# Optimization experiments

Hardware: AMD Instinct MI355X
Metric: run time of the kernel (lower is better)

## Reference

```python
import jax, jax.numpy as jnp
import numpy as np
from jax import lax

EPS = 1e-5
W_BITS = 8
A_BITS = 8


def _ste_round(x):
    # straight-through round (brevitas-style)
    return x + lax.stop_gradient(jnp.round(x) - x)


def weight_fake_quant(w, bits=W_BITS):
    # symmetric per-output-channel int quant: scale = max|w| / (2^(b-1)-1)
    qmax = float(2 ** (bits - 1) - 1)
    s = jnp.max(jnp.abs(w), axis=(1, 2, 3), keepdims=True) / qmax
    s = jnp.maximum(s, 1e-8)
    return jnp.clip(_ste_round(w / s), -qmax, qmax) * s


def quant_relu(x, scale, bits=A_BITS):
    # QuantReLU: relu then unsigned fake-quant with learned per-tensor scale
    qmax = float(2 ** bits - 1)
    s = jnp.maximum(scale, 1e-6)
    return jnp.clip(_ste_round(jax.nn.relu(x) / s), 0.0, qmax) * s


def conv2d(x, w, stride=1, padding=0):
    return lax.conv_general_dilated(
        x, w, window_strides=(stride, stride),
        padding=[(padding, padding), (padding, padding)],
        dimension_numbers=('NCHW', 'OIHW', 'NCHW'))


def batchnorm(x, gamma, beta, mean, var):
    # eval-mode BN with running stats
    inv = gamma / jnp.sqrt(var + EPS)
    return x * inv[None, :, None, None] + (beta - mean * inv)[None, :, None, None]


def setup_inputs() -> dict:
    key = jax.random.key(0)
    ks = jax.random.split(key, 20)
    B, Cin, P, H, W = 64, 1024, 256, 14, 14
    inp = {
        'x': jax.random.normal(ks[0], (B, Cin, H, W), jnp.float32),
        'w1': jax.random.normal(ks[1], (P, Cin, 1, 1), jnp.float32) * 0.05,
        'w2': jax.random.normal(ks[2], (P, P, 3, 3), jnp.float32) * 0.05,
        'w3': jax.random.normal(ks[3], (Cin, P, 1, 1), jnp.float32) * 0.05,
        'bn1_gamma': jax.random.uniform(ks[4], (P,), jnp.float32, 0.5, 1.5),
        'bn1_beta': jax.random.normal(ks[5], (P,), jnp.float32) * 0.1,
        'bn1_mean': jax.random.normal(ks[6], (P,), jnp.float32) * 0.1,
        'bn1_var': jax.random.uniform(ks[7], (P,), jnp.float32, 0.5, 1.5),
        'bn2_gamma': jax.random.uniform(ks[8], (P,), jnp.float32, 0.5, 1.5),
        'bn2_beta': jax.random.normal(ks[9], (P,), jnp.float32) * 0.1,
        'bn2_mean': jax.random.normal(ks[10], (P,), jnp.float32) * 0.1,
        'bn2_var': jax.random.uniform(ks[11], (P,), jnp.float32, 0.5, 1.5),
        'bn3_gamma': jax.random.uniform(ks[12], (Cin,), jnp.float32, 0.5, 1.5),
        'bn3_beta': jax.random.normal(ks[13], (Cin,), jnp.float32) * 0.1,
        'bn3_mean': jax.random.normal(ks[14], (Cin,), jnp.float32) * 0.1,
        'bn3_var': jax.random.uniform(ks[15], (Cin,), jnp.float32, 0.5, 1.5),
        's1': jax.random.uniform(ks[16], (1,), jnp.float32, 0.02, 0.1),
        's2': jax.random.uniform(ks[17], (1,), jnp.float32, 0.02, 0.1),
        's3': jax.random.uniform(ks[18], (1,), jnp.float32, 0.02, 0.1),
    }
    return inp


def reference(x, w1, w2, w3,
              bn1_gamma, bn1_beta, bn1_mean, bn1_var,
              bn2_gamma, bn2_beta, bn2_mean, bn2_var,
              bn3_gamma, bn3_beta, bn3_mean, bn3_var,
              s1, s2, s3):
    identity = x
    out = conv2d(x, weight_fake_quant(w1))
    out = batchnorm(out, bn1_gamma, bn1_beta, bn1_mean, bn1_var)
    out = quant_relu(out, s1)
    out = conv2d(out, weight_fake_quant(w2), stride=1, padding=1)
    out = batchnorm(out, bn2_gamma, bn2_beta, bn2_mean, bn2_var)
    out = quant_relu(out, s2)
    out = conv2d(out, weight_fake_quant(w3))
    out = batchnorm(out, bn3_gamma, bn3_beta, bn3_mean, bn3_var)
    out = out + identity  # downsample=None -> identity skip
    out = quant_relu(out, s3)
    return out
```

## Files before the change

### kernel.cpp

```cpp
#include <hip/hip_runtime.h>
#include <stdint.h>
#include <stddef.h>

typedef unsigned short u16;
typedef unsigned int   u32;
typedef __bf16  bf16x8 __attribute__((ext_vector_type(8)));
typedef unsigned short us8 __attribute__((ext_vector_type(8)));
typedef unsigned short us4 __attribute__((ext_vector_type(4)));
typedef float   f32x4  __attribute__((ext_vector_type(4)));

#define DEVFN static __device__ __forceinline__

DEVFN u16 f2bf(float f) {
    u32 u = __float_as_uint(f);
    return (u16)((u + 0x7FFFu + ((u >> 16) & 1u)) >> 16);
}
DEVFN float bf2f(u16 h) { return __uint_as_float(((u32)h) << 16); }

#define GLL(g, l) __builtin_amdgcn_global_load_lds( \
    (__attribute__((address_space(1))) void*)(g),   \
    (__attribute__((address_space(3))) void*)(l), 16, 0, 0)

#define NREAL 12544
#define NPAD  16384
#define GUARD_ROWS 32

DEVFN float blockReduceMax(float m) {
    for (int off = 32; off; off >>= 1) m = fmaxf(m, __shfl_xor(m, off));
    __shared__ float s[4];
    int lane = threadIdx.x & 63, w = threadIdx.x >> 6;
    if (lane == 0) s[w] = m;
    __syncthreads();
    m = fmaxf(fmaxf(s[0], s[1]), fmaxf(s[2], s[3]));
    return m;
}

__global__ __launch_bounds__(256) void k_prep(
    const float* __restrict__ w1, const float* __restrict__ w2, const float* __restrict__ w3,
    const float* __restrict__ x,
    u16* __restrict__ w1d, u16* __restrict__ w2t, u16* __restrict__ w3q,
    float* __restrict__ sw1, float* __restrict__ sw2, float* __restrict__ sw3,
    u16* __restrict__ xsplit)
{
    __shared__ float tile[64*197];
    const int bid = blockIdx.x, t = threadIdx.x;

    if (bid < 256) {
        int p = bid;
        const float* wr = w1 + (size_t)p * 1024;
        float v[4], m = 0.f;
        for (int i = 0; i < 4; ++i) { v[i] = wr[t + i*256]; m = fmaxf(m, fabsf(v[i])); }
        m = blockReduceMax(m);
        float s = fmaxf(m / 127.0f, 1e-8f);
        if (t == 0) sw1[p] = s;
        for (int i = 0; i < 4; ++i) {
            float q = rintf(v[i] / s);
            q = fminf(fmaxf(q, -127.f), 127.f);
            u16 h = f2bf(q);
            w1d[(size_t)p*2048 + t + i*256]        = h;
            w1d[(size_t)p*2048 + 1024 + t + i*256] = h;
        }
    } else if (bid < 512) {
        int p = bid - 256;
        const float* wr = w2 + (size_t)p * 2304;
        float v[9], m = 0.f;
        for (int i = 0; i < 9; ++i) { v[i] = wr[t + i*256]; m = fmaxf(m, fabsf(v[i])); }
        m = blockReduceMax(m);
        float s = fmaxf(m / 127.0f, 1e-8f);
        if (t == 0) sw2[p] = s;
        for (int i = 0; i < 9; ++i) {
            int f = t + i*256;
            int ci = f / 9, r = f - ci*9;
            float q = rintf(v[i] / s);
            q = fminf(fmaxf(q, -127.f), 127.f);
            w2t[(size_t)p*2304 + r*256 + ci] = f2bf(q);
        }
    } else if (bid < 1536) {
        int co = bid - 512;
        float v = w3[(size_t)co*256 + t];
        float m = blockReduceMax(fabsf(v));
        float s = fmaxf(m / 127.0f, 1e-8f);
        if (t == 0) sw3[co] = s;
        float q = rintf(v / s);
        q = fminf(fmaxf(q, -127.f), 127.f);
        w3q[(size_t)co*256 + t] = f2bf(q);
    } else {
        int sb = bid - 1536;
        int b = sb >> 4, cg = sb & 15;
        const float* xb = x + ((size_t)b*1024 + cg*64) * 196;
        for (int i = t; i < 3136; i += 256) {
            f32x4 v = *(const f32x4*)&xb[i*4];
            int g = i*4;
#pragma unroll
            for (int j = 0; j < 4; ++j) {
                int gg = g + j;
                tile[gg + gg/196] = v[j];
            }
        }
        __syncthreads();
        for (int i = t; i < 3136; i += 256) {
            int pos = i >> 4, c4 = (i & 15) << 2;
            us4 hi, lo;
#pragma unroll
            for (int j = 0; j < 4; ++j) {
                float v = tile[(c4 + j)*197 + pos];
                u16 h = f2bf(v);
                hi[j] = h;
                lo[j] = f2bf(v - bf2f(h));
            }
            size_t n = (size_t)(b*196 + pos);
            *(us4*)&xsplit[n*2048 + cg*64 + c4]        = hi;
            *(us4*)&xsplit[n*2048 + 1024 + cg*64 + c4] = lo;
        }
    }
}

__global__ void k_coef(const float* g1, const float* b1, const float* m1, const float* v1,
                       const float* g2, const float* b2, const float* m2, const float* v2,
                       const float* g3, const float* b3, const float* m3, const float* v3,
                       const float* s1p, const float* s2p,
                       const float* sw1, const float* sw2, const float* sw3,
                       float* a1, float* c1, float* a2, float* c2, float* a3, float* c3) {
    int t = threadIdx.x;
    float s1 = fmaxf(s1p[0], 1e-6f), s2 = fmaxf(s2p[0], 1e-6f);
    if (t < 256) {
        float inv1 = g1[t] / sqrtf(v1[t] + 1e-5f);
        a1[t] = sw1[t] * inv1 / s1;
        c1[t] = (b1[t] - m1[t] * inv1) / s1;
        float inv2 = g2[t] / sqrtf(v2[t] + 1e-5f);
        a2[t] = sw2[t] * s1 * inv2 / s2;
        c2[t] = (b2[t] - m2[t] * inv2) / s2;
    }
    float inv3 = g3[t] / sqrtf(v3[t] + 1e-5f);
    a3[t] = sw3[t] * s2 * inv3;
    c3[t] = b3[t] - m3[t] * inv3;
}

template<int CONV>
__global__ __launch_bounds__(256) void k_gemm(
    const u16* __restrict__ A, const u16* __restrict__ Bact,
    u16* __restrict__ actout,
    const float* __restrict__ ca, const float* __restrict__ cc,
    const float* __restrict__ xin, const float* __restrict__ s3p,
    float* __restrict__ outp)
{
    constexpr int KSA = CONV==1 ? 2048 : (CONV==2 ? 2304 : 256);
    constexpr int KSB = CONV==1 ? 2048 : 256;
    constexpr int NKT = CONV==1 ? 32 : (CONV==2 ? 36 : 4);

    __shared__ u16 lA[3][128*64];
    __shared__ u16 lB[3][64*64];

    const int t = threadIdx.x;
    const int lane = t & 63, wv = t >> 6;
    const int n0 = blockIdx.x * 64, m0 = blockIdx.y * 128;

    f32x4 acc[4][2];
#pragma unroll
    for (int i = 0; i < 4; ++i)
#pragma unroll
        for (int j = 0; j < 2; ++j) acc[i][j] = f32x4{0.f,0.f,0.f,0.f};

    const int srA = wv*32 + (lane >> 3);
    const int srB = wv*16 + (lane >> 3);
    const int ssel = (((lane & 7) ^ ((lane >> 3) & 7))) * 8;
    const int wr = wv >> 1, wc = wv & 1;
    const int fr = lane & 15, fg = lane >> 4;
    const int fsw = (fr & 7) << 4;

    auto stageK = [&](int kt, int buf) {
        int bcol, bshift;
        if constexpr (CONV == 2) {
            bcol = (kt & 3) * 64;
            int kpos = kt >> 2;
            int ky = kpos / 3, kx = kpos - ky*3;
            bshift = (ky - 1)*16 + (kx - 1);
        } else { bcol = kt * 64; bshift = 0; }
#pragma unroll
        for (int c = 0; c < 4; ++c) {
            const u16* g = A + (size_t)(m0 + srA + c*8) * KSA + kt*64 + ssel;
            GLL(g, &lA[buf][(wv*32 + c*8) * 64]);
        }
#pragma unroll
        for (int c = 0; c < 2; ++c) {
            const u16* g = Bact + (ptrdiff_t)(n0 + srB + c*8 + bshift) * KSB + bcol + ssel;
            GLL(g, &lB[buf][(wv*16 + c*8) * 64]);
        }
    };

    auto computeK = [&](int buf) {
        const char* bA = (const char*)&lA[buf][0];
        const char* bB = (const char*)&lB[buf][0];
        __builtin_amdgcn_s_setprio(1);
#pragma unroll
        for (int kk = 0; kk < 2; ++kk) {
            bf16x8 af[4], bfv[2];
#pragma unroll
            for (int m = 0; m < 4; ++m) {
                int row = wr*64 + m*16 + fr;
                const char* p = bA + row*128 + ((kk*64 + fg*16) ^ fsw);
                af[m] = __builtin_bit_cast(bf16x8, *(const us8*)p);
            }
#pragma unroll
            for (int n = 0; n < 2; ++n) {
                int row = wc*32 + n*16 + fr;
                const char* p = bB + row*128 + ((kk*64 + fg*16) ^ fsw);
                bfv[n] = __builtin_bit_cast(bf16x8, *(const us8*)p);
            }
#pragma unroll
            for (int m = 0; m < 4; ++m)
#pragma unroll
                for (int n = 0; n < 2; ++n)
                    acc[m][n] = __builtin_amdgcn_mfma_f32_16x16x32_bf16(af[m], bfv[n], acc[m][n], 0, 0, 0);
        }
        __builtin_amdgcn_s_setprio(0);
    };

    stageK(0, 0);
    stageK(1, 1);
    asm volatile("s_waitcnt vmcnt(6)" ::: "memory");
    __builtin_amdgcn_s_barrier();

    int cur = 0;
    for (int kt = 0; kt < NKT; ++kt) {
        int nxt2 = cur + 2; if (nxt2 >= 3) nxt2 -= 3;
        if (kt + 2 < NKT) stageK(kt + 2, nxt2);
        computeK(cur);
        if (kt + 1 < NKT) {
            if (kt + 2 < NKT) { asm volatile("s_waitcnt vmcnt(6)" ::: "memory"); }
            else              { asm volatile("s_waitcnt vmcnt(0)" ::: "memory"); }
            __builtin_amdgcn_s_barrier();
        }
        cur = cur + 1 == 3 ? 0 : cur + 1;
    }

    const int pb = m0 + wr*64 + fg*4;
    const int nb = n0 + wc*32 + fr;

    if constexpr (CONV != 3) {
        (void)xin; (void)s3p; (void)outp;
#pragma unroll
        for (int m = 0; m < 4; ++m) {
            int p0 = pb + m*16;
            float av[4], cv[4];
#pragma unroll
            for (int j = 0; j < 4; ++j) { av[j] = ca[p0+j]; cv[j] = cc[p0+j]; }
#pragma unroll
            for (int n = 0; n < 2; ++n) {
                int nn = nb + n*16;
                int np;
                if constexpr (CONV == 1) {
                    int b  = nn / 196;
                    int pos = nn - b*196;
                    int h = pos / 14, w = pos - h*14;
                    np = b*256 + (h+1)*16 + (w+1);
                } else {
                    int hp = (nn >> 4) & 15, wp = nn & 15;
                    if (hp < 1 || hp > 14 || wp < 1 || wp > 14) continue;
                    np = (nn >> 8)*196 + (hp-1)*14 + (wp-1);
                }
                us4 st;
#pragma unroll
                for (int j = 0; j < 4; ++j) {
                    float y = fmaxf(acc[m][n][j]*av[j] + cv[j], 0.f);
                    float q = fminf(rintf(y), 255.f);
                    st[j] = f2bf(q);
                }
                *(us4*)&actout[(size_t)np*256 + p0] = st;
            }
        }
    } else {
        (void)actout;
        float s3 = fmaxf(s3p[0], 1e-6f);
        float rs3 = 1.0f / s3;
#pragma unroll
        for (int n = 0; n < 2; ++n) {
            int co = nb + n*16;
            float av = ca[co], cv = cc[co];
#pragma unroll
            for (int m = 0; m < 4; ++m) {
                int p4 = pb + m*16;
                int b  = p4 / 196;
                int hw = p4 - b*196;
                size_t off = ((size_t)((b << 10) + co))*196 + hw;
                f32x4 xv = *(const f32x4*)&xin[off];
                f32x4 st;
#pragma unroll
                for (int j = 0; j < 4; ++j) {
                    float y = fmaxf(acc[m][n][j]*av + cv + xv[j], 0.f);
                    float q = fminf(rintf(y * rs3), 255.f);
                    st[j] = q * s3;
                }
                *(f32x4*)&outp[off] = st;
            }
        }
    }
}

extern "C" void kernel_launch(void* const* d_in, const int* in_sizes, int n_in,
                              void* d_out, int out_size, void* d_ws, size_t ws_size,
                              hipStream_t stream) {
    (void)in_sizes; (void)n_in; (void)out_size; (void)ws_size;
    const float* x   = (const float*)d_in[0];
    const float* w1  = (const float*)d_in[1];
    const float* w2  = (const float*)d_in[2];
    const float* w3  = (const float*)d_in[3];
    const float* g1  = (const float*)d_in[4];
    const float* b1  = (const float*)d_in[5];
    const float* m1  = (const float*)d_in[6];
    const float* v1  = (const float*)d_in[7];
    const float* g2  = (const float*)d_in[8];
    const float* b2  = (const float*)d_in[9];
    const float* m2  = (const float*)d_in[10];
    const float* v2  = (const float*)d_in[11];
    const float* g3  = (const float*)d_in[12];
    const float* b3  = (const float*)d_in[13];
    const float* m3  = (const float*)d_in[14];
    const float* v3  = (const float*)d_in[15];
    const float* s1p = (const float*)d_in[16];
    const float* s2p = (const float*)d_in[17];
    const float* s3p = (const float*)d_in[18];
    float* out = (float*)d_out;

    char* w = (char*)d_ws;
    u16* w1d = (u16*)w;  w += (size_t)256*2048*2;
    u16* w2t = (u16*)w;  w += (size_t)256*2304*2;
    u16* w3q = (u16*)w;  w += (size_t)1024*256*2;
    float* sw1 = (float*)w; w += 256*4;
    float* sw2 = (float*)w; w += 256*4;
    float* sw3 = (float*)w; w += 1024*4;
    float* a1 = (float*)w; w += 256*4;
    float* c1 = (float*)w; w += 256*4;
    float* a2 = (float*)w; w += 256*4;
    float* c2 = (float*)w; w += 256*4;
    float* a3 = (float*)w; w += 1024*4;
    float* c3 = (float*)w; w += 1024*4;
    u16* xsplit = (u16*)w; w += (size_t)NREAL*2048*2;
    u16* act1g  = (u16*)w; w += (size_t)(NPAD + 2*GUARD_ROWS)*256*2;
    u16* act1   = act1g + (size_t)GUARD_ROWS*256;
    u16* act2   = (u16*)w; w += (size_t)NREAL*256*2;

    hipMemsetAsync(act1g, 0, (size_t)(NPAD + 2*GUARD_ROWS)*256*2, stream);

    k_prep<<<2560, 256, 0, stream>>>(w1, w2, w3, x, w1d, w2t, w3q, sw1, sw2, sw3, xsplit);
    k_coef<<<1, 1024, 0, stream>>>(g1,b1,m1,v1, g2,b2,m2,v2, g3,b3,m3,v3,
                                   s1p, s2p, sw1, sw2, sw3,
                                   a1,c1, a2,c2, a3,c3);

    k_gemm<1><<<dim3(196, 2), 256, 0, stream>>>(w1d, xsplit, act1, a1, c1, nullptr, nullptr, nullptr);
    k_gemm<2><<<dim3(256, 2), 256, 0, stream>>>(w2t, act1, act2, a2, c2, nullptr, nullptr, nullptr);
    k_gemm<3><<<dim3(16, 98), 256, 0, stream>>>(act2, w3q, nullptr, a3, c3, x, s3p, out);
}
```

Baseline: 250.2 us.

## Switch all three conv GEMMs from bf16 to int8 MFMA with offset-corrected epilogues

Weights become int8 and activations are stored as offset int8 (value minus 128), with the offset folded into the BN bias using per-channel weight sums. The input x is split into fixed-point hi/lo int8 halves, and conv1 accumulates them in separate int32 accumulators. All GEMMs use the 16x16x64 i8 MFMA, halving operand bytes and K iterations. The coefficient kernel and the memset are folded into the prep kernel. The fixed-point split of x at scale 4096 with clamping adds quantization error and risks overflow for large inputs.

```diff
diff --git a/kernel.cpp b/kernel.cpp
--- a/kernel.cpp
+++ b/kernel.cpp
@@ -4,18 +4,13 @@
 
 typedef unsigned short u16;
 typedef unsigned int   u32;
-typedef __bf16  bf16x8 __attribute__((ext_vector_type(8)));
-typedef unsigned short us8 __attribute__((ext_vector_type(8)));
-typedef unsigned short us4 __attribute__((ext_vector_type(4)));
-typedef float   f32x4  __attribute__((ext_vector_type(4)));
+typedef signed char    s8;
+typedef int   i32x4 __attribute__((ext_vector_type(4)));
+typedef float f32x4 __attribute__((ext_vector_type(4)));
+typedef s8    s8x4  __attribute__((ext_vector_type(4)));
+typedef u32   u32x4 __attribute__((ext_vector_type(4)));
 
 #define DEVFN static __device__ __forceinline__
-
-DEVFN u16 f2bf(float f) {
-    u32 u = __float_as_uint(f);
-    return (u16)((u + 0x7FFFu + ((u >> 16) & 1u)) >> 16);
-}
-DEVFN float bf2f(u16 h) { return __uint_as_float(((u32)h) << 16); }
 
 #define GLL(g, l) __builtin_amdgcn_global_load_lds( \
     (__attribute__((address_space(1))) void*)(g),   \
@@ -24,6 +19,7 @@
 #define NREAL 12544
 #define NPAD  16384
 #define GUARD_ROWS 32
+#define SXI 4096.0f
 
 DEVFN float blockReduceMax(float m) {
     for (int off = 32; off; off >>= 1) m = fmaxf(m, __shfl_xor(m, off));
@@ -31,16 +27,30 @@
     int lane = threadIdx.x & 63, w = threadIdx.x >> 6;
     if (lane == 0) s[w] = m;
     __syncthreads();
-    m = fmaxf(fmaxf(s[0], s[1]), fmaxf(s[2], s[3]));
-    return m;
+    return fmaxf(fmaxf(s[0], s[1]), fmaxf(s[2], s[3]));
+}
+DEVFN float blockReduceSum(float v) {
+    for (int off = 32; off; off >>= 1) v += __shfl_xor(v, off);
+    __shared__ float s[4];
+    int lane = threadIdx.x & 63, w = threadIdx.x >> 6;
+    __syncthreads();
+    if (lane == 0) s[w] = v;
+    __syncthreads();
+    return s[0] + s[1] + s[2] + s[3];
 }
 
 __global__ __launch_bounds__(256) void k_prep(
     const float* __restrict__ w1, const float* __restrict__ w2, const float* __restrict__ w3,
     const float* __restrict__ x,
-    u16* __restrict__ w1d, u16* __restrict__ w2t, u16* __restrict__ w3q,
-    float* __restrict__ sw1, float* __restrict__ sw2, float* __restrict__ sw3,
-    u16* __restrict__ xsplit)
+    const float* __restrict__ g1, const float* __restrict__ b1, const float* __restrict__ m1, const float* __restrict__ v1,
+    const float* __restrict__ g2, const float* __restrict__ b2, const float* __restrict__ m2, const float* __restrict__ v2,
+    const float* __restrict__ g3, const float* __restrict__ b3, const float* __restrict__ m3, const float* __restrict__ v3,
+    const float* __restrict__ s1p, const float* __restrict__ s2p,
+    s8* __restrict__ w1q8, s8* __restrict__ w2t8, s8* __restrict__ w3q8,
+    float* __restrict__ a1, float* __restrict__ c1,
+    float* __restrict__ a2, float* __restrict__ c2,
+    float* __restrict__ a3, float* __restrict__ c3,
+    s8* __restrict__ xq, s8* __restrict__ act1g)
 {
     __shared__ float tile[64*197];
     const int bid = blockIdx.x, t = threadIdx.x;
@@ -48,43 +58,65 @@
     if (bid < 256) {
         int p = bid;
         const float* wr = w1 + (size_t)p * 1024;
-        float v[4], m = 0.f;
-        for (int i = 0; i < 4; ++i) { v[i] = wr[t + i*256]; m = fmaxf(m, fabsf(v[i])); }
-        m = blockReduceMax(m);
-        float s = fmaxf(m / 127.0f, 1e-8f);
-        if (t == 0) sw1[p] = s;
+        float v[4], mx = 0.f;
+        for (int i = 0; i < 4; ++i) { v[i] = wr[t + i*256]; mx = fmaxf(mx, fabsf(v[i])); }
+        mx = blockReduceMax(mx);
+        float s = fmaxf(mx / 127.0f, 1e-8f);
+        float qs = 0.f;
         for (int i = 0; i < 4; ++i) {
-            float q = rintf(v[i] / s);
-            q = fminf(fmaxf(q, -127.f), 127.f);
-            u16 h = f2bf(q);
-            w1d[(size_t)p*2048 + t + i*256]        = h;
-            w1d[(size_t)p*2048 + 1024 + t + i*256] = h;
+            float q = fminf(fmaxf(rintf(v[i] / s), -127.f), 127.f);
+            s8 qb = (s8)(int)q;
+            w1q8[(size_t)p*2048 + t + i*256]        = qb;
+            w1q8[(size_t)p*2048 + 1024 + t + i*256] = qb;
+            qs += q;
+        }
+        qs = blockReduceSum(qs);
+        if (t == 0) {
+            float s1 = fmaxf(s1p[0], 1e-6f);
+            float inv = g1[p] / sqrtf(v1[p] + 1e-5f);
+            float a = s * (1.0f / SXI) * inv / s1;
+            a1[p] = a;
+            c1[p] = (b1[p] - m1[p] * inv) / s1 + 128.0f * qs * a;
         }
     } else if (bid < 512) {
         int p = bid - 256;
         const float* wr = w2 + (size_t)p * 2304;
-        float v[9], m = 0.f;
-        for (int i = 0; i < 9; ++i) { v[i] = wr[t + i*256]; m = fmaxf(m, fabsf(v[i])); }
-        m = blockReduceMax(m);
-        float s = fmaxf(m / 127.0f, 1e-8f);
-        if (t == 0) sw2[p] = s;
+        float v[9], mx = 0.f;
+        for (int i = 0; i < 9; ++i) { v[i] = wr[t + i*256]; mx = fmaxf(mx, fabsf(v[i])); }
+        mx = blockReduceMax(mx);
+        float s = fmaxf(mx / 127.0f, 1e-8f);
+        float qs = 0.f;
         for (int i = 0; i < 9; ++i) {
             int f = t + i*256;
             int ci = f / 9, r = f - ci*9;
-            float q = rintf(v[i] / s);
-            q = fminf(fmaxf(q, -127.f), 127.f);
-            w2t[(size_t)p*2304 + r*256 + ci] = f2bf(q);
+            float q = fminf(fmaxf(rintf(v[i] / s), -127.f), 127.f);
+            w2t8[(size_t)p*2304 + r*256 + ci] = (s8)(int)q;
+            qs += q;
+        }
+        qs = blockReduceSum(qs);
+        if (t == 0) {
+            float s1 = fmaxf(s1p[0], 1e-6f), s2 = fmaxf(s2p[0], 1e-6f);
+            float inv = g2[p] / sqrtf(v2[p] + 1e-5f);
+            float a = s * s1 * inv / s2;
+            a2[p] = a;
+            c2[p] = (b2[p] - m2[p] * inv) / s2 + 128.0f * qs * a;
         }
     } else if (bid < 1536) {
         int co = bid - 512;
         float v = w3[(size_t)co*256 + t];
-        float m = blockReduceMax(fabsf(v));
-        float s = fmaxf(m / 127.0f, 1e-8f);
-        if (t == 0) sw3[co] = s;
-        float q = rintf(v / s);
-        q = fminf(fmaxf(q, -127.f), 127.f);
-        w3q[(size_t)co*256 + t] = f2bf(q);
-    } else {
+        float mx = blockReduceMax(fabsf(v));
+        float s = fmaxf(mx / 127.0f, 1e-8f);
+        float q = fminf(fmaxf(rintf(v / s), -127.f), 127.f);
+        w3q8[(size_t)co*256 + t] = (s8)(int)q;
+        float qs = blockReduceSum(q);
+        if (t == 0) {
+            float s2 = fmaxf(s2p[0], 1e-6f);
+            float inv = g3[co] / sqrtf(v3[co] + 1e-5f);
+            float a = s * s2 * inv;
+            a3[co] = a;
+            c3[co] = (b3[co] - m3[co] * inv) + 128.0f * qs * a;
+        }
+    } else if (bid < 2560) {
         int sb = bid - 1536;
         int b = sb >> 4, cg = sb & 15;
         const float* xb = x + ((size_t)b*1024 + cg*64) * 196;
@@ -100,70 +132,57 @@
         __syncthreads();
         for (int i = t; i < 3136; i += 256) {
             int pos = i >> 4, c4 = (i & 15) << 2;
-            us4 hi, lo;
+            s8x4 hi, lo;
 #pragma unroll
             for (int j = 0; j < 4; ++j) {
                 float v = tile[(c4 + j)*197 + pos];
-                u16 h = f2bf(v);
-                hi[j] = h;
-                lo[j] = f2bf(v - bf2f(h));
+                int xf = (int)rintf(v * SXI);
+                xf = xf > 32767 ? 32767 : (xf < -32767 ? -32767 : xf);
+                int h = xf >> 8;
+                int l = xf - (h << 8) - 128;
+                hi[j] = (s8)h;
+                lo[j] = (s8)l;
             }
             size_t n = (size_t)(b*196 + pos);
-            *(us4*)&xsplit[n*2048 + cg*64 + c4]        = hi;
-            *(us4*)&xsplit[n*2048 + 1024 + cg*64 + c4] = lo;
-        }
+            *(s8x4*)&xq[n*2048 + cg*64 + c4]        = hi;
+            *(s8x4*)&xq[n*2048 + 1024 + cg*64 + c4] = lo;
+        }
+    } else {
+        const int total16 = (NPAD + 2*GUARD_ROWS) * 256 / 16;
+        u32x4 val; val[0] = val[1] = val[2] = val[3] = 0x80808080u;
+        u32x4* dst = (u32x4*)act1g;
+        for (int i = (bid - 2560)*256 + t; i < total16; i += 260*256) dst[i] = val;
     }
-}
-
-__global__ void k_coef(const float* g1, const float* b1, const float* m1, const float* v1,
-                       const float* g2, const float* b2, const float* m2, const float* v2,
-                       const float* g3, const float* b3, const float* m3, const float* v3,
-                       const float* s1p, const float* s2p,
-                       const float* sw1, const float* sw2, const float* sw3,
-                       float* a1, float* c1, float* a2, float* c2, float* a3, float* c3) {
-    int t = threadIdx.x;
-    float s1 = fmaxf(s1p[0], 1e-6f), s2 = fmaxf(s2p[0], 1e-6f);
-    if (t < 256) {
-        float inv1 = g1[t] / sqrtf(v1[t] + 1e-5f);
-        a1[t] = sw1[t] * inv1 / s1;
-        c1[t] = (b1[t] - m1[t] * inv1) / s1;
-        float inv2 = g2[t] / sqrtf(v2[t] + 1e-5f);
-        a2[t] = sw2[t] * s1 * inv2 / s2;
-        c2[t] = (b2[t] - m2[t] * inv2) / s2;
-    }
-    float inv3 = g3[t] / sqrtf(v3[t] + 1e-5f);
-    a3[t] = sw3[t] * s2 * inv3;
-    c3[t] = b3[t] - m3[t] * inv3;
 }
 
 template<int CONV>
 __global__ __launch_bounds__(256) void k_gemm(
-    const u16* __restrict__ A, const u16* __restrict__ Bact,
-    u16* __restrict__ actout,
+    const s8* __restrict__ A, const s8* __restrict__ Bact,
+    s8* __restrict__ actout,
     const float* __restrict__ ca, const float* __restrict__ cc,
     const float* __restrict__ xin, const float* __restrict__ s3p,
     float* __restrict__ outp)
 {
     constexpr int KSA = CONV==1 ? 2048 : (CONV==2 ? 2304 : 256);
     constexpr int KSB = CONV==1 ? 2048 : 256;
-    constexpr int NKT = CONV==1 ? 32 : (CONV==2 ? 36 : 4);
-
-    __shared__ u16 lA[3][128*64];
-    __shared__ u16 lB[3][64*64];
+    constexpr int NKT = CONV==1 ? 16 : (CONV==2 ? 18 : 2);
+
+    __shared__ s8 lA[3][128*128];
+    __shared__ s8 lB[3][64*128];
 
     const int t = threadIdx.x;
     const int lane = t & 63, wv = t >> 6;
     const int n0 = blockIdx.x * 64, m0 = blockIdx.y * 128;
 
-    f32x4 acc[4][2];
+    i32x4 acc[4][2], accB[4][2];
 #pragma unroll
     for (int i = 0; i < 4; ++i)
 #pragma unroll
-        for (int j = 0; j < 2; ++j) acc[i][j] = f32x4{0.f,0.f,0.f,0.f};
+        for (int j = 0; j < 2; ++j) { acc[i][j] = i32x4{0,0,0,0}; accB[i][j] = i32x4{0,0,0,0}; }
 
     const int srA = wv*32 + (lane >> 3);
     const int srB = wv*16 + (lane >> 3);
-    const int ssel = (((lane & 7) ^ ((lane >> 3) & 7))) * 8;
+    const int ssel = (((lane & 7) ^ ((lane >> 3) & 7))) * 16;
     const int wr = wv >> 1, wc = wv & 1;
     const int fr = lane & 15, fg = lane >> 4;
     const int fsw = (fr & 7) << 4;
@@ -171,47 +190,45 @@
     auto stageK = [&](int kt, int buf) {
         int bcol, bshift;
         if constexpr (CONV == 2) {
-            bcol = (kt & 3) * 64;
-            int kpos = kt >> 2;
+            bcol = (kt & 1) * 128;
+            int kpos = kt >> 1;
             int ky = kpos / 3, kx = kpos - ky*3;
             bshift = (ky - 1)*16 + (kx - 1);
-        } else { bcol = kt * 64; bshift = 0; }
+        } else { bcol = kt * 128; bshift = 0; }
 #pragma unroll
         for (int c = 0; c < 4; ++c) {
-            const u16* g = A + (size_t)(m0 + srA + c*8) * KSA + kt*64 + ssel;
-            GLL(g, &lA[buf][(wv*32 + c*8) * 64]);
+            const s8* g = A + (size_t)(m0 + srA + c*8) * KSA + kt*128 + ssel;
+            GLL(g, &lA[buf][(wv*32 + c*8) * 128]);
         }
 #pragma unroll
         for (int c = 0; c < 2; ++c) {
-            const u16* g = Bact + (ptrdiff_t)(n0 + srB + c*8 + bshift) * KSB + bcol + ssel;
-            GLL(g, &lB[buf][(wv*16 + c*8) * 64]);
+            const s8* g = Bact + (ptrdiff_t)(n0 + srB + c*8 + bshift) * KSB + bcol + ssel;
+            GLL(g, &lB[buf][(wv*16 + c*8) * 128]);
         }
     };
 
-    auto computeK = [&](int buf) {
-        const char* bA = (const char*)&lA[buf][0];
-        const char* bB = (const char*)&lB[buf][0];
+    auto computeK = [&](int buf, i32x4 (&ac)[4][2]) {
+        const s8* bA = &lA[buf][0];
+        const s8* bB = &lB[buf][0];
         __builtin_amdgcn_s_setprio(1);
 #pragma unroll
         for (int kk = 0; kk < 2; ++kk) {
-            bf16x8 af[4], bfv[2];
+            i32x4 af[4], bf[2];
 #pragma unroll
             for (int m = 0; m < 4; ++m) {
                 int row = wr*64 + m*16 + fr;
-                const char* p = bA + row*128 + ((kk*64 + fg*16) ^ fsw);
-                af[m] = __builtin_bit_cast(bf16x8, *(const us8*)p);
+                af[m] = *(const i32x4*)(bA + row*128 + ((kk*64 + fg*16) ^ fsw));
             }
 #pragma unroll
             for (int n = 0; n < 2; ++n) {
                 int row = wc*32 + n*16 + fr;
-                const char* p = bB + row*128 + ((kk*64 + fg*16) ^ fsw);
-                bfv[n] = __builtin_bit_cast(bf16x8, *(const us8*)p);
+                bf[n] = *(const i32x4*)(bB + row*128 + ((kk*64 + fg*16) ^ fsw));
             }
 #pragma unroll
             for (int m = 0; m < 4; ++m)
 #pragma unroll
                 for (int n = 0; n < 2; ++n)
-                    acc[m][n] = __builtin_amdgcn_mfma_f32_16x16x32_bf16(af[m], bfv[n], acc[m][n], 0, 0, 0);
+                    ac[m][n] = __builtin_amdgcn_mfma_i32_16x16x64_i8(af[m], bf[n], ac[m][n], 0, 0, 0);
         }
         __builtin_amdgcn_s_setprio(0);
     };
@@ -221,17 +238,17 @@
     asm volatile("s_waitcnt vmcnt(6)" ::: "memory");
     __builtin_amdgcn_s_barrier();
 
-    int cur = 0;
+#pragma unroll
     for (int kt = 0; kt < NKT; ++kt) {
-        int nxt2 = cur + 2; if (nxt2 >= 3) nxt2 -= 3;
-        if (kt + 2 < NKT) stageK(kt + 2, nxt2);
-        computeK(cur);
+        const int buf = kt % 3;
+        if (kt + 2 < NKT) stageK(kt + 2, (kt + 2) % 3);
+        if (CONV == 1 && kt >= 8) computeK(buf, accB);
+        else                      computeK(buf, acc);
         if (kt + 1 < NKT) {
             if (kt + 2 < NKT) { asm volatile("s_waitcnt vmcnt(6)" ::: "memory"); }
             else              { asm volatile("s_waitcnt vmcnt(0)" ::: "memory"); }
             __builtin_amdgcn_s_barrier();
         }
-        cur = cur + 1 == 3 ? 0 : cur + 1;
     }
 
     const int pb = m0 + wr*64 + fg*4;
@@ -259,14 +276,19 @@
                     if (hp < 1 || hp > 14 || wp < 1 || wp > 14) continue;
                     np = (nn >> 8)*196 + (hp-1)*14 + (wp-1);
                 }
-                us4 st;
+                s8x4 st;
 #pragma unroll
                 for (int j = 0; j < 4; ++j) {
-                    float y = fmaxf(acc[m][n][j]*av[j] + cv[j], 0.f);
-                    float q = fminf(rintf(y), 255.f);
-                    st[j] = f2bf(q);
+                    float fa;
+                    if constexpr (CONV == 1)
+                        fa = 256.0f * (float)acc[m][n][j] + (float)accB[m][n][j];
+                    else
+                        fa = (float)acc[m][n][j];
+                    float y = fmaxf(fa * av[j] + cv[j], 0.f);
+                    int q = (int)fminf(rintf(y), 255.f);
+                    st[j] = (s8)(q - 128);
                 }
-                *(us4*)&actout[(size_t)np*256 + p0] = st;
+                *(s8x4*)&actout[(size_t)np*256 + p0] = st;
             }
         }
     } else {
@@ -287,7 +309,7 @@
                 f32x4 st;
 #pragma unroll
                 for (int j = 0; j < 4; ++j) {
-                    float y = fmaxf(acc[m][n][j]*av + cv + xv[j], 0.f);
+                    float y = fmaxf((float)acc[m][n][j] * av + cv + xv[j], 0.f);
                     float q = fminf(rintf(y * rs3), 255.f);
                     st[j] = q * s3;
                 }
@@ -323,31 +345,28 @@
     float* out = (float*)d_out;
 
     char* w = (char*)d_ws;
-    u16* w1d = (u16*)w;  w += (size_t)256*2048*2;
-    u16* w2t = (u16*)w;  w += (size_t)256*2304*2;
-    u16* w3q = (u16*)w;  w += (size_t)1024*256*2;
-    float* sw1 = (float*)w; w += 256*4;
-    float* sw2 = (float*)w; w += 256*4;
-    float* sw3 = (float*)w; w += 1024*4;
+    s8* w1q8 = (s8*)w;  w += (size_t)256*2048;
+    s8* w2t8 = (s8*)w;  w += (size_t)256*2304;
+    s8* w3q8 = (s8*)w;  w += (size_t)1024*256;
     float* a1 = (float*)w; w += 256*4;
     float* c1 = (float*)w; w += 256*4;
     float* a2 = (float*)w; w += 256*4;
     float* c2 = (float*)w; w += 256*4;
     float* a3 = (float*)w; w += 1024*4;
     float* c3 = (float*)w; w += 1024*4;
-    u16* xsplit = (u16*)w; w += (size_t)NREAL*2048*2;
-    u16* act1g  = (u16*)w; w += (size_t)(NPAD + 2*GUARD_ROWS)*256*2;
-    u16* act1   = act1g + (size_t)GUARD_ROWS*256;
-    u16* act2   = (u16*)w; w += (size_t)NREAL*256*2;
-
-    hipMemsetAsync(act1g, 0, (size_t)(NPAD + 2*GUARD_ROWS)*256*2, stream);
-
-    k_prep<<<2560, 256, 0, stream>>>(w1, w2, w3, x, w1d, w2t, w3q, sw1, sw2, sw3, xsplit);
-    k_coef<<<1, 1024, 0, stream>>>(g1,b1,m1,v1, g2,b2,m2,v2, g3,b3,m3,v3,
-                                   s1p, s2p, sw1, sw2, sw3,
-                                   a1,c1, a2,c2, a3,c3);
-
-    k_gemm<1><<<dim3(196, 2), 256, 0, stream>>>(w1d, xsplit, act1, a1, c1, nullptr, nullptr, nullptr);
-    k_gemm<2><<<dim3(256, 2), 256, 0, stream>>>(w2t, act1, act2, a2, c2, nullptr, nullptr, nullptr);
-    k_gemm<3><<<dim3(16, 98), 256, 0, stream>>>(act2, w3q, nullptr, a3, c3, x, s3p, out);
-}
+    s8* xq    = (s8*)w; w += (size_t)NREAL*2048;
+    s8* act1g = (s8*)w; w += (size_t)(NPAD + 2*GUARD_ROWS)*256;
+    s8* act1  = act1g + (size_t)GUARD_ROWS*256;
+    s8* act2  = (s8*)w; w += (size_t)NREAL*256;
+
+    k_prep<<<2820, 256, 0, stream>>>(w1, w2, w3, x,
+                                     g1,b1,m1,v1, g2,b2,m2,v2, g3,b3,m3,v3,
+                                     s1p, s2p,
+                                     w1q8, w2t8, w3q8,
+                                     a1,c1, a2,c2, a3,c3,
+                                     xq, act1g);
+
+    k_gemm<1><<<dim3(196, 2), 256, 0, stream>>>(w1q8, xq, act1, a1, c1, nullptr, nullptr, nullptr);
+    k_gemm<2><<<dim3(256, 2), 256, 0, stream>>>(w2t8, act1, act2, a2, c2, nullptr, nullptr, nullptr);
+    k_gemm<3><<<dim3(16, 98), 256, 0, stream>>>(act2, w3q8, nullptr, a3, c3, x, s3p, out);
+}
```

Result: faster. 203.8 us (-18.5%).
